# Optimization experiments

Hardware: AMD Instinct MI355X
Metric: run time of the kernel (lower is better)

## Reference

```python
import jax, jax.numpy as jnp
import numpy as np

N = 100000   # nodes
E = 1600000  # edges (avg degree 16)
IN = 128     # in_channels
H = 256      # hidden_channels
L = 3        # num_layers
C = 2        # num_classes
EPS = 1e-5   # BatchNorm eps


def setup_inputs() -> dict:
    key = jax.random.key(0)
    ks = jax.random.split(key, 8)
    s = 0.05
    x = jax.random.normal(ks[0], (N, IN), jnp.float32)
    edge_index = jax.random.randint(ks[1], (2, E), 0, N)
    return dict(
        x=x,
        edge_index=edge_index,
        proj_w=jax.random.normal(ks[2], (IN, H), jnp.float32) * s,
        proj_b=jnp.zeros((H,), jnp.float32),
        lin_l_w=jax.random.normal(ks[3], (L, H, H), jnp.float32) * s,
        lin_l_b=jnp.zeros((L, H), jnp.float32),
        lin_r_w=jax.random.normal(ks[4], (L, H, H), jnp.float32) * s,
        bn_g=jnp.ones((L, H), jnp.float32),
        bn_b=jnp.zeros((L, H), jnp.float32),
        fc1_w=jax.random.normal(ks[5], (H, H // 2), jnp.float32) * s,
        fc1_b=jnp.zeros((H // 2,), jnp.float32),
        fc2_w=jax.random.normal(ks[6], (H // 2, C), jnp.float32) * s,
        fc2_b=jnp.zeros((C,), jnp.float32),
    )


def reference(x, edge_index, proj_w, proj_b, lin_l_w, lin_l_b, lin_r_w,
              bn_g, bn_b, fc1_w, fc1_b, fc2_w, fc2_b):
    src, dst = edge_index[0], edge_index[1]
    # in-degree for mean aggregation (SAGEConv aggr='mean')
    deg = jax.ops.segment_sum(jnp.ones((E,), x.dtype), dst, num_segments=N)
    inv_deg = (1.0 / jnp.maximum(deg, 1.0))[:, None]  # [N,1]

    h = jax.nn.relu(x @ proj_w + proj_b)  # [N,H]; dropout is identity in eval
    for i in range(L):
        # SAGEConv: lin_l(mean_{j in N(i)} h_j) + lin_r(h_i)
        agg = jax.ops.segment_sum(h[src], dst, num_segments=N) * inv_deg  # [N,H]
        out = agg @ lin_l_w[i] + lin_l_b[i] + h @ lin_r_w[i]
        # BatchNorm over nodes (batch statistics, biased variance)
        mu = out.mean(axis=0)
        var = out.var(axis=0)
        out = (out - mu) * jax.lax.rsqrt(var + EPS) * bn_g[i] + bn_b[i]
        out = jax.nn.relu(out)
        h = out + h if i > 0 else out  # residual from layer 1 onward

    embeddings = h
    z = jax.nn.relu(embeddings @ fc1_w + fc1_b)
    logits = z @ fc2_w + fc2_b
    return (logits, embeddings)
```

## Files before the change

### kernel.cpp

```cpp
#include <hip/hip_runtime.h>
#include <stdint.h>

#define NN 100000
#define NE 1600000
#define INC 128
#define HID 256
#define MP  100096
#define NBK 391
#define EPB 2048

typedef unsigned short u16;
typedef __attribute__((ext_vector_type(2))) float f32x2;
typedef __attribute__((ext_vector_type(4))) float f32x4;
typedef __attribute__((ext_vector_type(8))) short s16x8;

static __device__ __forceinline__ float bf2f(u16 u){
  union { uint32_t i; float f; } v; v.i = ((uint32_t)u) << 16; return v.f;
}
static __device__ __forceinline__ u16 f2bf(float f){
  union { float f; uint32_t i; } v; v.f = f;
  uint32_t r = v.i + 0x7FFFu + ((v.i >> 16) & 1u);
  return (u16)(r >> 16);
}
static __device__ __forceinline__ void up8(uint4 o, float* v){
  v[0]=bf2f((u16)(o.x&0xffffu)); v[1]=bf2f((u16)(o.x>>16));
  v[2]=bf2f((u16)(o.y&0xffffu)); v[3]=bf2f((u16)(o.y>>16));
  v[4]=bf2f((u16)(o.z&0xffffu)); v[5]=bf2f((u16)(o.z>>16));
  v[6]=bf2f((u16)(o.w&0xffffu)); v[7]=bf2f((u16)(o.w>>16));
}
static __device__ __forceinline__ uint4 pk8(const float* v){
  uint4 o;
  o.x = (uint32_t)f2bf(v[0]) | ((uint32_t)f2bf(v[1])<<16);
  o.y = (uint32_t)f2bf(v[2]) | ((uint32_t)f2bf(v[3])<<16);
  o.z = (uint32_t)f2bf(v[4]) | ((uint32_t)f2bf(v[5])<<16);
  o.w = (uint32_t)f2bf(v[6]) | ((uint32_t)f2bf(v[7])<<16);
  return o;
}
static __device__ __forceinline__ uint2 pkf8(const float* r){
  uint32_t lo = __builtin_amdgcn_cvt_pk_fp8_f32(r[0], r[1], 0u, false);
  lo = __builtin_amdgcn_cvt_pk_fp8_f32(r[2], r[3], lo, true);
  uint32_t hi = __builtin_amdgcn_cvt_pk_fp8_f32(r[4], r[5], 0u, false);
  hi = __builtin_amdgcn_cvt_pk_fp8_f32(r[6], r[7], hi, true);
  return make_uint2(lo, hi);
}

static __device__ __forceinline__ void gload16(const void* g, void* l){
  __builtin_amdgcn_global_load_lds((const __attribute__((address_space(1))) void*)g,
                                   (__attribute__((address_space(3))) void*)l, 16, 0, 0);
}


__global__ __launch_bounds__(256) void zero_k(float* bnacc, int* bcnt){
  int i = blockIdx.x*256 + threadIdx.x;
  if (i < 3*8192) bnacc[i] = 0.f;
  if (i < NBK) bcnt[i] = 0;
}

__global__ __launch_bounds__(256) void cvt_k(const float* __restrict__ src, u16* __restrict__ dst, int n4){
  int i = blockIdx.x*256 + threadIdx.x;
  if (i >= n4) return;
  float4 v = ((const float4*)src)[i];
  uint2 o;
  o.x = (uint32_t)f2bf(v.x) | ((uint32_t)f2bf(v.y)<<16);
  o.y = (uint32_t)f2bf(v.z) | ((uint32_t)f2bf(v.w)<<16);
  ((uint2*)dst)[i] = o;
}

__global__ __launch_bounds__(256) void cvt8_k(const uint4* __restrict__ h, uint2* __restrict__ h8, int n){
  int i = blockIdx.x*256 + threadIdx.x;
  if (i >= n) return;
  float v[8];
  up8(h[i], v);
  h8[i] = pkf8(v);
}

__global__ __launch_bounds__(256) void pack_k(const float* __restrict__ src, u16* __restrict__ dst,
                                              int K, int NC, int ksoff){
  int t = blockIdx.x*256 + threadIdx.x;
  if (t >= K*NC) return;
  int k = t / NC, n = t % NC;
  int NT = NC >> 4;
  int ks = ksoff + (k >> 5);
  int l  = ((k >> 3) & 3)*16 + (n & 15);
  int j  = k & 7;
  dst[((size_t)(ks*NT + (n>>4))*64 + l)*8 + j] = f2bf(src[(size_t)k*NC + n]);
}


__global__ __launch_bounds__(256) void bhist_k(const int* __restrict__ ei, int* __restrict__ bcnt){
  __shared__ int h[NBK];
  for (int i = threadIdx.x; i < NBK; i += 256) h[i] = 0;
  __syncthreads();
  int e0 = blockIdx.x * EPB;
  #pragma unroll
  for (int j = 0; j < EPB/256; ++j){
    int e = e0 + j*256 + threadIdx.x;
    if (e < NE) atomicAdd(&h[ei[NE + e] >> 8], 1);
  }
  __syncthreads();
  for (int i = threadIdx.x; i < NBK; i += 256)
    if (h[i]) atomicAdd(&bcnt[i], h[i]);
}

__global__ __launch_bounds__(512) void bscan_k(const int* __restrict__ bcnt, int* __restrict__ bcur){
  __shared__ int sd[512];
  int t = threadIdx.x;
  int v = (t < NBK) ? bcnt[t] : 0;
  sd[t] = v; __syncthreads();
  for (int o = 1; o < 512; o <<= 1){
    int x = (t >= o) ? sd[t-o] : 0;
    __syncthreads();
    sd[t] += x;
    __syncthreads();
  }
  if (t < NBK) bcur[t] = sd[t] - v;
}

__global__ __launch_bounds__(256) void bfill_k(const int* __restrict__ ei, int* __restrict__ bcur,
                                               uint2* __restrict__ epair){
  __shared__ int cnt[NBK];
  __shared__ int gb[NBK];
  for (int i = threadIdx.x; i < NBK; i += 256) cnt[i] = 0;
  __syncthreads();
  int e0 = blockIdx.x * EPB;
  int srcv[EPB/256], dstv[EPB/256], rnk[EPB/256];
  #pragma unroll
  for (int j = 0; j < EPB/256; ++j){
    int e = e0 + j*256 + threadIdx.x;
    if (e < NE){
      srcv[j] = ei[e];
      dstv[j] = ei[NE + e];
      rnk[j]  = atomicAdd(&cnt[dstv[j] >> 8], 1);
    } else dstv[j] = -1;
  }
  __syncthreads();
  for (int i = threadIdx.x; i < NBK; i += 256){
    int c = cnt[i];
    gb[i] = c ? atomicAdd(&bcur[i], c) : 0;
  }
  __syncthreads();
  #pragma unroll
  for (int j = 0; j < EPB/256; ++j){
    if (dstv[j] >= 0)
      epair[gb[dstv[j] >> 8] + rnk[j]] = make_uint2((unsigned)srcv[j], (unsigned)dstv[j]);
  }
}

__global__ __launch_bounds__(256) void csort_k(const uint2* __restrict__ epair,
                                               const int* __restrict__ bcnt, const int* __restrict__ bcur,
                                               int* __restrict__ ci, int* __restrict__ rp){
  __shared__ int hist[256], pfx[256], cnt2[256];
  int b = blockIdx.x, t = threadIdx.x;
  int cnt  = bcnt[b];
  int base = bcur[b] - cnt;
  hist[t] = 0; cnt2[t] = 0;
  __syncthreads();
  for (int e = t; e < cnt; e += 256)
    atomicAdd(&hist[epair[base + e].y & 255u], 1);
  __syncthreads();
  int v = hist[t];
  pfx[t] = v;
  __syncthreads();
  for (int o = 1; o < 256; o <<= 1){
    int x = (t >= o) ? pfx[t - o] : 0;
    __syncthreads();
    pfx[t] += x;
    __syncthreads();
  }
  int node = b*256 + t;
  if (node < NN) rp[node] = base + pfx[t] - v;
  if (b == NBK-1 && t == 0) rp[NN] = NE;
  for (int e = t; e < cnt; e += 256){
    uint2 p = epair[base + e];
    int ld = (int)(p.y & 255u);
    int r  = atomicAdd(&cnt2[ld], 1);
    ci[base + pfx[ld] - hist[ld] + r] = (int)p.x;
  }
}


__global__ __launch_bounds__(256) void agg8_k(const int* __restrict__ rp, const int* __restrict__ ci,
                                              const uint4* __restrict__ h8, u16* __restrict__ ag){
  int wid  = (int)((blockIdx.x*256u + threadIdx.x) >> 6);
  int lane = threadIdx.x & 63;
  int ql   = lane & 15;
  int w    = wid*4 + (lane >> 4);
  bool act = (w < NN);
  int e0 = 0, e1 = 0;
  if (act){ e0 = rp[w]; e1 = rp[w+1]; }
  int cnt = e1 - e0;

  float a[16];
  #pragma unroll
  for (int k = 0; k < 16; ++k) a[k] = 0.f;

  for (int base = 0; __any(base < cnt); base += 16){
    int rem = cnt - base;
    int my = 0;
    if (ql < rem) my = ci[e0 + base + ql];
    for (int j0 = 0; j0 < 16 && __any(j0 < rem); j0 += 4){
      uint4 v[4];
      #pragma unroll
      for (int jj = 0; jj < 4; ++jj){
        int j = j0 + jj;
        int s = __shfl(my, (lane & 48) + j);
        v[jj] = make_uint4(0,0,0,0);
        if (j < rem) v[jj] = h8[(size_t)s*16 + ql];
      }
      #pragma unroll
      for (int jj = 0; jj < 4; ++jj){
        uint32_t wd[4] = {v[jj].x, v[jj].y, v[jj].z, v[jj].w};
        #pragma unroll
        for (int p = 0; p < 4; ++p){
          f32x2 lo = __builtin_amdgcn_cvt_pk_f32_fp8(wd[p], false);
          f32x2 hi = __builtin_amdgcn_cvt_pk_f32_fp8(wd[p], true);
          a[p*4+0] += lo[0]; a[p*4+1] += lo[1];
          a[p*4+2] += hi[0]; a[p*4+3] += hi[1];
        }
      }
    }
  }

  if (act){
    float inv = 1.0f / (float)(cnt > 0 ? cnt : 1);
    float r0[8], r1[8];
    #pragma unroll
    for (int k = 0; k < 8; ++k){ r0[k] = a[k]*inv; r1[k] = a[8+k]*inv; }
    uint4* agu = (uint4*)ag;
    agu[(size_t)w*32 + ql*2]     = pk8(r0);
    agu[(size_t)w*32 + ql*2 + 1] = pk8(r1);
  }
}


__global__ __launch_bounds__(256) void aggb_k(const int* __restrict__ rp, const int* __restrict__ ci,
                                              const u16* __restrict__ h, u16* __restrict__ ag){
  int w = (int)((blockIdx.x*256u + threadIdx.x) >> 6);
  int lane = threadIdx.x & 63;
  if (w >= NN) return;
  int e0 = rp[w], e1 = rp[w+1];
  const uint2* hu = (const uint2*)h;
  float a0=0.f, a1=0.f, a2=0.f, a3=0.f;
  for (int base = e0; base < e1; base += 64){
    int cnt = e1 - base; if (cnt > 64) cnt = 64;
    int my = ci[base + (lane < cnt ? lane : cnt-1)];
    int i = 0;
    for (; i + 4 <= cnt; i += 4){
      int s0 = __builtin_amdgcn_readlane(my, i);
      int s1 = __builtin_amdgcn_readlane(my, i+1);
      int s2 = __builtin_amdgcn_readlane(my, i+2);
      int s3 = __builtin_amdgcn_readlane(my, i+3);
      uint2 v0 = hu[(size_t)s0*64 + lane];
      uint2 v1 = hu[(size_t)s1*64 + lane];
      uint2 v2 = hu[(size_t)s2*64 + lane];
      uint2 v3 = hu[(size_t)s3*64 + lane];
      a0 += bf2f((u16)(v0.x&0xffffu)) + bf2f((u16)(v1.x&0xffffu)) + bf2f((u16)(v2.x&0xffffu)) + bf2f((u16)(v3.x&0xffffu));
      a1 += bf2f((u16)(v0.x>>16))     + bf2f((u16)(v1.x>>16))     + bf2f((u16)(v2.x>>16))     + bf2f((u16)(v3.x>>16));
      a2 += bf2f((u16)(v0.y&0xffffu)) + bf2f((u16)(v1.y&0xffffu)) + bf2f((u16)(v2.y&0xffffu)) + bf2f((u16)(v3.y&0xffffu));
      a3 += bf2f((u16)(v0.y>>16))     + bf2f((u16)(v1.y>>16))     + bf2f((u16)(v2.y>>16))     + bf2f((u16)(v3.y>>16));
    }
    for (; i < cnt; ++i){
      int s0 = __builtin_amdgcn_readlane(my, i);
      uint2 v = hu[(size_t)s0*64 + lane];
      a0 += bf2f((u16)(v.x&0xffffu));
      a1 += bf2f((u16)(v.x>>16));
      a2 += bf2f((u16)(v.y&0xffffu));
      a3 += bf2f((u16)(v.y>>16));
    }
  }
  int d = e1 - e0;
  float inv = 1.0f / (float)(d > 0 ? d : 1);
  uint2 o;
  o.x = (uint32_t)f2bf(a0*inv) | ((uint32_t)f2bf(a1*inv) << 16);
  o.y = (uint32_t)f2bf(a2*inv) | ((uint32_t)f2bf(a3*inv) << 16);
  ((uint2*)ag)[(size_t)w*64 + lane] = o;
}


template<int KS1, int KS2, int NCC, int EPI>
__global__ __launch_bounds__(256, 3) void gemm3_k(
    const u16* __restrict__ A1, const u16* __restrict__ A2,
    const u16* __restrict__ Wp, const float* __restrict__ bias,
    u16* __restrict__ Cout, int M, float* __restrict__ stS)
{
  constexpr int NT    = NCC >> 4;
  constexpr int NFRAG = NCC / 64;
  constexpr int NS1   = KS1 / 2;
  constexpr int NSTEP = (KS1 + KS2) / 2;

  __shared__ u16 Al[2][64*64];

  const int t    = threadIdx.x;
  const int lane = t & 63;
  const int wv   = t >> 6;
  const int r15  = lane & 15, kg = lane >> 4;
  const int rb   = blockIdx.x * 64;
  const int nt0w = wv * NFRAG;

  f32x4 acc[4][NFRAG];
  #pragma unroll
  for (int m = 0; m < 4; ++m)
    #pragma unroll
    for (int n = 0; n < NFRAG; ++n){ f32x4 z = {0.f,0.f,0.f,0.f}; acc[m][n] = z; }

  auto stageA = [&](int step, int bsel){
    const bool inA1 = (step < NS1);
    const u16* Ab   = inA1 ? A1 : A2;
    const int  Krow = (inA1 ? KS1 : KS2) * 32;
    const int  kloc = (inA1 ? step : step - NS1) * 64;
    #pragma unroll
    for (int c = 0; c < 2; ++c){
      int row = c*32 + wv*8 + (lane >> 3);
      int gc  = (lane & 7) ^ (row & 7);
      const u16* g = Ab + (size_t)(rb + row)*Krow + kloc + gc*8;
      gload16(g, &Al[bsel][c*2048 + wv*512]);
    }
  };
  auto loadB = [&](int ss, s16x8* dst){
    const u16* g = Wp + ((size_t)(ss*NT + nt0w)*64 + lane)*8;
    #pragma unroll
    for (int n = 0; n < NFRAG; ++n)
      dst[n] = *(const s16x8*)(g + (size_t)n*512);
  };

  s16x8 bb[2][NFRAG];
  stageA(0, 0);
  loadB(0, bb[0]);
  __syncthreads();

  #pragma unroll
  for (int step = 0; step < NSTEP; ++step){
    const int cur = step & 1;
    if (step + 1 < NSTEP) stageA(step + 1, cur ^ 1);
    #pragma unroll
    for (int sl = 0; sl < 2; ++sl){
      const int ss = step*2 + sl;
      const int p  = ss & 1;
      if (ss + 1 < NSTEP*2) loadB(ss + 1, bb[p ^ 1]);
      s16x8 af[4];
      const char* Ab = (const char*)&Al[cur][0];
      #pragma unroll
      for (int m = 0; m < 4; ++m){
        int row = m*16 + r15;
        int c16 = (sl*4 + kg) ^ (row & 7);
        af[m] = *(const s16x8*)(Ab + row*128 + c16*16);
      }
      #pragma unroll
      for (int m = 0; m < 4; ++m)
        #pragma unroll
        for (int n = 0; n < NFRAG; ++n)
          acc[m][n] = __builtin_amdgcn_mfma_f32_16x16x32_bf16(af[m], bb[p][n], acc[m][n], 0, 0, 0);
    }
    __syncthreads();
  }

  #pragma unroll
  for (int n = 0; n < NFRAG; ++n){
    int col = (nt0w + n)*16 + r15;
    float bc = bias[col];
    float s = 0.f, q = 0.f;
    #pragma unroll
    for (int m = 0; m < 4; ++m){
      int rbase = rb + m*16 + kg*4;
      #pragma unroll
      for (int r = 0; r < 4; ++r){
        int row = rbase + r;
        float val = acc[m][n][r] + bc;
        if (EPI == 0) val = fmaxf(val, 0.f);
        bool ok = row < M;
        if (ok) Cout[(size_t)row*NCC + col] = f2bf(val);
        if (EPI == 1 && ok){ s += val; q += val*val; }
      }
    }
    if (EPI == 1){
      s += __shfl_xor(s, 16); s += __shfl_xor(s, 32);
      q += __shfl_xor(q, 16); q += __shfl_xor(q, 32);
      if (lane < 16){
        int idx = ((blockIdx.x & 15) << 9) + col;
        atomicAdd(&stS[idx], s);
        atomicAdd(&stS[idx + 256], q);
      }
    }
  }
}


__global__ __launch_bounds__(256) void bnfin_k(const float* __restrict__ acc,
                                               const float* __restrict__ g, const float* __restrict__ b,
                                               float* __restrict__ coef){
  int c = threadIdx.x;
  float s = 0.f, q = 0.f;
  #pragma unroll
  for (int j = 0; j < 16; ++j){
    s += acc[j*512 + c];
    q += acc[j*512 + 256 + c];
  }
  float mean = s * (1.0f / (float)NN);
  float var  = q * (1.0f / (float)NN) - mean*mean;
  float sc = g[c] * rsqrtf(var + 1e-5f);
  coef[c] = sc;
  coef[256 + c] = b[c] - mean*sc;
}

__global__ __launch_bounds__(256) void bnapply_k(const uint4* __restrict__ outb, uint4* __restrict__ h,
                                                 uint2* __restrict__ h8,
                                                 const float* __restrict__ coef, int layer, int wr8){
  int i = blockIdx.x*256 + threadIdx.x;
  if (i >= NN*32) return;
  int col0 = (i & 31) * 8;
  const float4* scp = (const float4*)(coef + col0);
  const float4* shp = (const float4*)(coef + 256 + col0);
  float4 s0 = scp[0], s1 = scp[1], t0 = shp[0], t1 = shp[1];
  float sc[8] = {s0.x,s0.y,s0.z,s0.w,s1.x,s1.y,s1.z,s1.w};
  float sh[8] = {t0.x,t0.y,t0.z,t0.w,t1.x,t1.y,t1.z,t1.w};
  float v[8], r[8];
  up8(outb[i], v);
  #pragma unroll
  for (int j = 0; j < 8; ++j) r[j] = fmaxf(v[j]*sc[j] + sh[j], 0.f);
  if (layer > 0){
    float hv[8];
    up8(h[i], hv);
    #pragma unroll
    for (int j = 0; j < 8; ++j) r[j] += hv[j];
  }
  h[i] = pk8(r);
  if (wr8) h8[i] = pkf8(r);
}


__global__ __launch_bounds__(256) void fc2_k(const u16* __restrict__ z, const float* __restrict__ w2,
                                             const float* __restrict__ b2, float* __restrict__ out){
  int w = (int)((blockIdx.x*256u + threadIdx.x) >> 6);
  int lane = threadIdx.x & 63;
  if (w >= NN) return;
  const uint32_t* zu = (const uint32_t*)(z + (size_t)w*128);
  uint32_t p = zu[lane];
  float z0 = bf2f((u16)(p & 0xffffu));
  float z1 = bf2f((u16)(p >> 16));
  float4 wv = ((const float4*)w2)[lane];
  float p0 = z0*wv.x + z1*wv.z;
  float p1 = z0*wv.y + z1*wv.w;
  #pragma unroll
  for (int off = 1; off < 64; off <<= 1){
    p0 += __shfl_xor(p0, off);
    p1 += __shfl_xor(p1, off);
  }
  if (lane == 0){
    out[(size_t)w*2]     = p0 + b2[0];
    out[(size_t)w*2 + 1] = p1 + b2[1];
  }
}

__global__ __launch_bounds__(256) void emb_k(const u16* __restrict__ h, float* __restrict__ out, int n4){
  int i = blockIdx.x*256 + threadIdx.x;
  if (i >= n4) return;
  uint2 v = ((const uint2*)h)[i];
  float4 o;
  o.x = bf2f((u16)(v.x & 0xffffu));
  o.y = bf2f((u16)(v.x >> 16));
  o.z = bf2f((u16)(v.y & 0xffffu));
  o.w = bf2f((u16)(v.y >> 16));
  ((float4*)out)[i] = o;
}


extern "C" void kernel_launch(void* const* d_in, const int* in_sizes, int n_in,
                              void* d_out, int out_size, void* d_ws, size_t ws_size,
                              hipStream_t stream){
  const float* x       = (const float*)d_in[0];
  const int*   ei      = (const int*)d_in[1];
  const float* proj_w  = (const float*)d_in[2];
  const float* proj_b  = (const float*)d_in[3];
  const float* lin_l_w = (const float*)d_in[4];
  const float* lin_l_b = (const float*)d_in[5];
  const float* lin_r_w = (const float*)d_in[6];
  const float* bn_g    = (const float*)d_in[7];
  const float* bn_b    = (const float*)d_in[8];
  const float* fc1_w   = (const float*)d_in[9];
  const float* fc1_b   = (const float*)d_in[10];
  const float* fc2_w   = (const float*)d_in[11];
  const float* fc2_b   = (const float*)d_in[12];
  float* out = (float*)d_out;

  char* ws = (char*)d_ws;
  size_t off = 0;
  auto alloc = [&](size_t b){ size_t o = off; off = (off + b + 255) & ~(size_t)255; return o; };

  u16* bufA    = (u16*)(ws + alloc((size_t)MP*256*2));
  u16* hbuf    = (u16*)(ws + alloc((size_t)MP*256*2));
  u16* bufC    = (u16*)(ws + alloc((size_t)MP*256*2));
  uint8_t* h8  = (uint8_t*)(ws + alloc((size_t)MP*256));
  u16* wp_proj = (u16*)(ws + alloc((size_t)4*16*64*8*2));
  u16* wp_l[3];
  for (int i = 0; i < 3; ++i) wp_l[i] = (u16*)(ws + alloc((size_t)16*16*64*8*2));
  u16* wp_fc1  = (u16*)(ws + alloc((size_t)8*8*64*8*2));
  int* rp    = (int*)(ws + alloc((size_t)(NN+1)*4));
  int* ci    = (int*)(ws + alloc((size_t)NE*4));
  int* bcnt  = (int*)(ws + alloc(NBK*4));
  int* bcur  = (int*)(ws + alloc(NBK*4));
  float* bnacc = (float*)(ws + alloc(3*8192*4));
  float* coef  = (float*)(ws + alloc(3*512*4));
  uint2* epair = (uint2*)bufC;
  (void)ws_size; (void)in_sizes; (void)n_in; (void)out_size;

  const int BFB = (NE + EPB - 1)/EPB;
  const int GX = MP/64;

  zero_k<<<96, 256, 0, stream>>>(bnacc, bcnt);

  bhist_k<<<BFB, 256, 0, stream>>>(ei, bcnt);
  bscan_k<<<1, 512, 0, stream>>>(bcnt, bcur);
  bfill_k<<<BFB, 256, 0, stream>>>(ei, bcur, epair);
  csort_k<<<NBK, 256, 0, stream>>>(epair, bcnt, bcur, ci, rp);

  cvt_k<<<(NN*INC/4 + 255)/256, 256, 0, stream>>>(x, bufA, NN*INC/4);
  pack_k<<<(128*256 + 255)/256, 256, 0, stream>>>(proj_w, wp_proj, 128, 256, 0);
  for (int i = 0; i < 3; ++i){
    pack_k<<<(256*256 + 255)/256, 256, 0, stream>>>(lin_l_w + (size_t)i*65536, wp_l[i], 256, 256, 0);
    pack_k<<<(256*256 + 255)/256, 256, 0, stream>>>(lin_r_w + (size_t)i*65536, wp_l[i], 256, 256, 8);
  }
  pack_k<<<(256*128 + 255)/256, 256, 0, stream>>>(fc1_w, wp_fc1, 256, 128, 0);

  gemm3_k<4,0,256,0><<<GX, 256, 0, stream>>>(bufA, nullptr, wp_proj, proj_b,
                                             hbuf, NN, nullptr);
  cvt8_k<<<(NN*32 + 255)/256, 256, 0, stream>>>((const uint4*)hbuf, (uint2*)h8, NN*32);

  for (int i = 0; i < 3; ++i){
    if (i < 2)
      agg8_k<<<((NN + 3)/4*64 + 255)/256, 256, 0, stream>>>(rp, ci, (const uint4*)h8, bufA);
    else
      aggb_k<<<(NN + 3)/4, 256, 0, stream>>>(rp, ci, hbuf, bufA);
    gemm3_k<8,8,256,1><<<GX, 256, 0, stream>>>(bufA, hbuf, wp_l[i], lin_l_b + (size_t)i*256,
                                               bufC, NN, bnacc + i*8192);
    bnfin_k<<<1, 256, 0, stream>>>(bnacc + i*8192, bn_g + (size_t)i*256, bn_b + (size_t)i*256, coef + i*512);
    bnapply_k<<<(NN*32 + 255)/256, 256, 0, stream>>>((const uint4*)bufC, (uint4*)hbuf, (uint2*)h8,
                                                     coef + i*512, i, (i == 0) ? 1 : 0);
  }

  gemm3_k<8,0,128,0><<<GX, 256, 0, stream>>>(hbuf, nullptr, wp_fc1, fc1_b,
                                             bufA, NN, nullptr);
  fc2_k<<<(NN + 3)/4, 256, 0, stream>>>(bufA, fc2_w, fc2_b, out);
  emb_k<<<(NN*64 + 255)/256, 256, 0, stream>>>(hbuf, out + 200000, NN*64);
}
```

Baseline: 692.2 us.

## Pack edge pairs into 32 bits, deepen gather batches, fuse embedding output into BN apply

Edge pairs for the bucket sort are packed as src<<8 | local dst in a single 32-bit word, halving intermediate traffic in bfill and csort. Both aggregation kernels now issue 8 neighbor gathers per batch instead of 4 to raise memory-level parallelism, at the cost of more registers. The final layer's BN apply writes fp32 embeddings directly, removing the separate emb_k pass that re-read hbuf. The embeddings are now written from fp32 values before bf16 rounding, which slightly changes their numerics.

```diff
diff --git a/kernel.cpp b/kernel.cpp
--- a/kernel.cpp
+++ b/kernel.cpp
@@ -117,21 +117,24 @@
 }
 
 __global__ __launch_bounds__(256) void bfill_k(const int* __restrict__ ei, int* __restrict__ bcur,
-                                               uint2* __restrict__ epair){
+                                               unsigned* __restrict__ epair){
   __shared__ int cnt[NBK];
   __shared__ int gb[NBK];
   for (int i = threadIdx.x; i < NBK; i += 256) cnt[i] = 0;
   __syncthreads();
   int e0 = blockIdx.x * EPB;
-  int srcv[EPB/256], dstv[EPB/256], rnk[EPB/256];
+  unsigned pk[EPB/256];
+  int bkt[EPB/256], rnk[EPB/256];
   #pragma unroll
   for (int j = 0; j < EPB/256; ++j){
     int e = e0 + j*256 + threadIdx.x;
     if (e < NE){
-      srcv[j] = ei[e];
-      dstv[j] = ei[NE + e];
-      rnk[j]  = atomicAdd(&cnt[dstv[j] >> 8], 1);
-    } else dstv[j] = -1;
+      int s = ei[e];
+      int d = ei[NE + e];
+      bkt[j] = d >> 8;
+      pk[j]  = ((unsigned)s << 8) | (unsigned)(d & 255);
+      rnk[j] = atomicAdd(&cnt[bkt[j]], 1);
+    } else bkt[j] = -1;
   }
   __syncthreads();
   for (int i = threadIdx.x; i < NBK; i += 256){
@@ -141,12 +144,12 @@
   __syncthreads();
   #pragma unroll
   for (int j = 0; j < EPB/256; ++j){
-    if (dstv[j] >= 0)
-      epair[gb[dstv[j] >> 8] + rnk[j]] = make_uint2((unsigned)srcv[j], (unsigned)dstv[j]);
-  }
-}
-
-__global__ __launch_bounds__(256) void csort_k(const uint2* __restrict__ epair,
+    if (bkt[j] >= 0)
+      epair[gb[bkt[j]] + rnk[j]] = pk[j];
+  }
+}
+
+__global__ __launch_bounds__(256) void csort_k(const unsigned* __restrict__ epair,
                                                const int* __restrict__ bcnt, const int* __restrict__ bcur,
                                                int* __restrict__ ci, int* __restrict__ rp){
   __shared__ int hist[256], pfx[256], cnt2[256];
@@ -156,7 +159,7 @@
   hist[t] = 0; cnt2[t] = 0;
   __syncthreads();
   for (int e = t; e < cnt; e += 256)
-    atomicAdd(&hist[epair[base + e].y & 255u], 1);
+    atomicAdd(&hist[epair[base + e] & 255u], 1);
   __syncthreads();
   int v = hist[t];
   pfx[t] = v;
@@ -171,10 +174,10 @@
   if (node < NN) rp[node] = base + pfx[t] - v;
   if (b == NBK-1 && t == 0) rp[NN] = NE;
   for (int e = t; e < cnt; e += 256){
-    uint2 p = epair[base + e];
-    int ld = (int)(p.y & 255u);
+    unsigned p = epair[base + e];
+    int ld = (int)(p & 255u);
     int r  = atomicAdd(&cnt2[ld], 1);
-    ci[base + pfx[ld] - hist[ld] + r] = (int)p.x;
+    ci[base + pfx[ld] - hist[ld] + r] = (int)(p >> 8);
   }
 }
 
@@ -198,17 +201,19 @@
     int rem = cnt - base;
     int my = 0;
     if (ql < rem) my = ci[e0 + base + ql];
-    for (int j0 = 0; j0 < 16 && __any(j0 < rem); j0 += 4){
-      uint4 v[4];
-      #pragma unroll
-      for (int jj = 0; jj < 4; ++jj){
+    #pragma unroll
+    for (int j0 = 0; j0 < 16; j0 += 8){
+      if (!__any(j0 < rem)) break;
+      uint4 v[8];
+      #pragma unroll
+      for (int jj = 0; jj < 8; ++jj){
         int j = j0 + jj;
         int s = __shfl(my, (lane & 48) + j);
         v[jj] = make_uint4(0,0,0,0);
         if (j < rem) v[jj] = h8[(size_t)s*16 + ql];
       }
       #pragma unroll
-      for (int jj = 0; jj < 4; ++jj){
+      for (int jj = 0; jj < 8; ++jj){
         uint32_t wd[4] = {v[jj].x, v[jj].y, v[jj].z, v[jj].w};
         #pragma unroll
         for (int p = 0; p < 4; ++p){
@@ -245,19 +250,20 @@
     int cnt = e1 - base; if (cnt > 64) cnt = 64;
     int my = ci[base + (lane < cnt ? lane : cnt-1)];
     int i = 0;
-    for (; i + 4 <= cnt; i += 4){
-      int s0 = __builtin_amdgcn_readlane(my, i);
-      int s1 = __builtin_amdgcn_readlane(my, i+1);
-      int s2 = __builtin_amdgcn_readlane(my, i+2);
-      int s3 = __builtin_amdgcn_readlane(my, i+3);
-      uint2 v0 = hu[(size_t)s0*64 + lane];
-      uint2 v1 = hu[(size_t)s1*64 + lane];
-      uint2 v2 = hu[(size_t)s2*64 + lane];
-      uint2 v3 = hu[(size_t)s3*64 + lane];
-      a0 += bf2f((u16)(v0.x&0xffffu)) + bf2f((u16)(v1.x&0xffffu)) + bf2f((u16)(v2.x&0xffffu)) + bf2f((u16)(v3.x&0xffffu));
-      a1 += bf2f((u16)(v0.x>>16))     + bf2f((u16)(v1.x>>16))     + bf2f((u16)(v2.x>>16))     + bf2f((u16)(v3.x>>16));
-      a2 += bf2f((u16)(v0.y&0xffffu)) + bf2f((u16)(v1.y&0xffffu)) + bf2f((u16)(v2.y&0xffffu)) + bf2f((u16)(v3.y&0xffffu));
-      a3 += bf2f((u16)(v0.y>>16))     + bf2f((u16)(v1.y>>16))     + bf2f((u16)(v2.y>>16))     + bf2f((u16)(v3.y>>16));
+    for (; i + 8 <= cnt; i += 8){
+      int s[8];
+      #pragma unroll
+      for (int jj = 0; jj < 8; ++jj) s[jj] = __builtin_amdgcn_readlane(my, i + jj);
+      uint2 v[8];
+      #pragma unroll
+      for (int jj = 0; jj < 8; ++jj) v[jj] = hu[(size_t)s[jj]*64 + lane];
+      #pragma unroll
+      for (int jj = 0; jj < 8; ++jj){
+        a0 += bf2f((u16)(v[jj].x & 0xffffu));
+        a1 += bf2f((u16)(v[jj].x >> 16));
+        a2 += bf2f((u16)(v[jj].y & 0xffffu));
+        a3 += bf2f((u16)(v[jj].y >> 16));
+      }
     }
     for (; i < cnt; ++i){
       int s0 = __builtin_amdgcn_readlane(my, i);
@@ -404,7 +410,8 @@
 
 __global__ __launch_bounds__(256) void bnapply_k(const uint4* __restrict__ outb, uint4* __restrict__ h,
                                                  uint2* __restrict__ h8,
-                                                 const float* __restrict__ coef, int layer, int wr8){
+                                                 const float* __restrict__ coef, int layer, int wr8,
+                                                 float* __restrict__ embout){
   int i = blockIdx.x*256 + threadIdx.x;
   if (i >= NN*32) return;
   int col0 = (i & 31) * 8;
@@ -425,6 +432,12 @@
   }
   h[i] = pk8(r);
   if (wr8) h8[i] = pkf8(r);
+  if (embout){
+    int row = i >> 5;
+    float4* ep = (float4*)(embout + (size_t)row*256 + col0);
+    ep[0] = make_float4(r[0], r[1], r[2], r[3]);
+    ep[1] = make_float4(r[4], r[5], r[6], r[7]);
+  }
 }
 
 
@@ -449,18 +462,6 @@
     out[(size_t)w*2]     = p0 + b2[0];
     out[(size_t)w*2 + 1] = p1 + b2[1];
   }
-}
-
-__global__ __launch_bounds__(256) void emb_k(const u16* __restrict__ h, float* __restrict__ out, int n4){
-  int i = blockIdx.x*256 + threadIdx.x;
-  if (i >= n4) return;
-  uint2 v = ((const uint2*)h)[i];
-  float4 o;
-  o.x = bf2f((u16)(v.x & 0xffffu));
-  o.y = bf2f((u16)(v.x >> 16));
-  o.z = bf2f((u16)(v.y & 0xffffu));
-  o.w = bf2f((u16)(v.y >> 16));
-  ((float4*)out)[i] = o;
 }
 
 
@@ -500,7 +501,7 @@
   int* bcur  = (int*)(ws + alloc(NBK*4));
   float* bnacc = (float*)(ws + alloc(3*8192*4));
   float* coef  = (float*)(ws + alloc(3*512*4));
-  uint2* epair = (uint2*)bufC;
+  unsigned* epair = (unsigned*)bufC;
   (void)ws_size; (void)in_sizes; (void)n_in; (void)out_size;
 
   const int BFB = (NE + EPB - 1)/EPB;
@@ -534,11 +535,11 @@
                                                bufC, NN, bnacc + i*8192);
     bnfin_k<<<1, 256, 0, stream>>>(bnacc + i*8192, bn_g + (size_t)i*256, bn_b + (size_t)i*256, coef + i*512);
     bnapply_k<<<(NN*32 + 255)/256, 256, 0, stream>>>((const uint4*)bufC, (uint4*)hbuf, (uint2*)h8,
-                                                     coef + i*512, i, (i == 0) ? 1 : 0);
+                                                     coef + i*512, i, (i == 0) ? 1 : 0,
+                                                     (i == 2) ? (out + 200000) : nullptr);
   }
 
   gemm3_k<8,0,128,0><<<GX, 256, 0, stream>>>(hbuf, nullptr, wp_fc1, fc1_b,
                                              bufA, NN, nullptr);
   fc2_k<<<(NN + 3)/4, 256, 0, stream>>>(bufA, fc2_w, fc2_b, out);
-  emb_k<<<(NN*64 + 255)/256, 256, 0, stream>>>(hbuf, out + 200000, NN*64);
-}
+}
```

After: 689.1 us. No clear change (-0.4%).
